# Performance work log

Hardware: AMD Instinct MI355X
Metric: run time of the kernel (lower is better)

## Reference

```python
import jax, jax.numpy as jnp
import numpy as np

N_HEAD, MODEL_DIM, KEY_DIM, VALUE_DIM = 16, 1024, 64, 64
B, S = 4, 2048
EPS = 1e-5
TEMP = float(np.sqrt(KEY_DIM))


def setup_inputs() -> dict:
    key = jax.random.key(0)
    ks = jax.random.split(key, 12)
    d = {
        'query': jax.random.normal(ks[0], (B, S, MODEL_DIM), jnp.float32),
        'key':   jax.random.normal(ks[1], (B, S, MODEL_DIM), jnp.float32),
        'value': jax.random.normal(ks[2], (B, S, MODEL_DIM), jnp.float32),
        # projection weights stored as [in, out]
        'Wq': jax.random.normal(ks[3], (MODEL_DIM, N_HEAD * KEY_DIM), jnp.float32) * np.sqrt(2.0 / (MODEL_DIM + KEY_DIM)),
        'bq': jnp.zeros((N_HEAD * KEY_DIM,), jnp.float32),
        'Wk': jax.random.normal(ks[4], (MODEL_DIM, N_HEAD * KEY_DIM), jnp.float32) * np.sqrt(2.0 / (MODEL_DIM + KEY_DIM)),
        'bk': jnp.zeros((N_HEAD * KEY_DIM,), jnp.float32),
        'Wv': jax.random.normal(ks[5], (MODEL_DIM, N_HEAD * VALUE_DIM), jnp.float32) * np.sqrt(2.0 / (MODEL_DIM + VALUE_DIM)),
        'bv': jnp.zeros((N_HEAD * VALUE_DIM,), jnp.float32),
        'Wo': jax.random.normal(ks[6], (N_HEAD * VALUE_DIM, MODEL_DIM), jnp.float32) * np.sqrt(2.0 / (N_HEAD * VALUE_DIM + MODEL_DIM)),
        'bo': jnp.zeros((MODEL_DIM,), jnp.float32),
        'ln_gamma': jnp.ones((MODEL_DIM,), jnp.float32),
        'ln_beta': jnp.zeros((MODEL_DIM,), jnp.float32),
    }
    return d


def reference(query, key, value, Wq, bq, Wk, bk, Wv, bv, Wo, bo, ln_gamma, ln_beta):
    b, sq, _ = query.shape
    residual = query
    # QKV projections -> [B, S, H, D]
    q = (query @ Wq + bq).reshape(b, sq, N_HEAD, KEY_DIM)
    k = (key @ Wk + bk).reshape(b, key.shape[1], N_HEAD, KEY_DIM)
    v = (value @ Wv + bv).reshape(b, value.shape[1], N_HEAD, VALUE_DIM)
    # scaled dot-product attention (dropout inactive in eval)
    scores = jnp.einsum('bqhd,bkhd->bhqk', q, k) / TEMP
    attn = jax.nn.softmax(scores, axis=-1)
    out = jnp.einsum('bhqk,bkhd->bqhd', attn, v).reshape(b, sq, N_HEAD * VALUE_DIM)
    # output projection + residual + LayerNorm
    out = out @ Wo + bo + residual
    mu = jnp.mean(out, axis=-1, keepdims=True)
    var = jnp.var(out, axis=-1, keepdims=True)
    return (out - mu) * jax.lax.rsqrt(var + EPS) * ln_gamma + ln_beta
```

## Files before the change

### kernel.cpp

```cpp
#include <hip/hip_runtime.h>
#include <math.h>

#define MD 1024
#define NH 16
#define HD 64
#define BATCH 4
#define SEQ 2048

typedef __attribute__((ext_vector_type(8))) short short8;
typedef __attribute__((ext_vector_type(4))) short short4v;
typedef __attribute__((ext_vector_type(4))) float f32x4;
typedef __attribute__((ext_vector_type(2))) unsigned int uint2v;

#define GLOAD16(gp, lp) __builtin_amdgcn_global_load_lds( \
    (const __attribute__((address_space(1))) void*)(gp),  \
    (__attribute__((address_space(3))) void*)(lp), 16, 0, 0)

__device__ inline unsigned short f2b(float f) {
    unsigned u = __builtin_bit_cast(unsigned, f);
    unsigned r = (u + 0x7fffu + ((u >> 16) & 1u)) >> 16;
    return (unsigned short)r;
}
__device__ inline float b2f(unsigned short s) {
    return __builtin_bit_cast(float, ((unsigned)s) << 16);
}

__global__ __launch_bounds__(256)
void prep_kernel(const float* __restrict__ x0, const float* __restrict__ x1,
                 const float* __restrict__ x2, unsigned short* __restrict__ y0,
                 unsigned short* __restrict__ y1, unsigned short* __restrict__ y2,
                 int n,
                 const float* __restrict__ W0, const float* __restrict__ W1,
                 const float* __restrict__ W2, const float* __restrict__ W3,
                 unsigned short* __restrict__ T0, unsigned short* __restrict__ T1,
                 unsigned short* __restrict__ T2, unsigned short* __restrict__ T3)
{
    __shared__ __attribute__((aligned(16))) float T[64][68];
    const int tid = threadIdx.x;
    if (blockIdx.y < 3) {
        const float* x = (blockIdx.y == 0) ? x0 : (blockIdx.y == 1) ? x1 : x2;
        unsigned short* y = (blockIdx.y == 0) ? y0 : (blockIdx.y == 1) ? y1 : y2;
        int i = (blockIdx.x * 256 + tid) * 8;
        if (i >= n) return;
        f32x4 a = *(const f32x4*)(x + i);
        f32x4 b = *(const f32x4*)(x + i + 4);
        short8 o;
        o[0] = (short)f2b(a[0]); o[1] = (short)f2b(a[1]);
        o[2] = (short)f2b(a[2]); o[3] = (short)f2b(a[3]);
        o[4] = (short)f2b(b[0]); o[5] = (short)f2b(b[1]);
        o[6] = (short)f2b(b[2]); o[7] = (short)f2b(b[3]);
        *(short8*)(y + i) = o;
        return;
    }
    const int bx = blockIdx.x;
    if (bx >= 1024) return;
    const int z = bx >> 8, t = bx & 255;
    const int nt = t & 15, kt = t >> 4;
    const float* W = (z == 0) ? W0 : (z == 1) ? W1 : (z == 2) ? W2 : W3;
    unsigned short* WT = (z == 0) ? T0 : (z == 1) ? T1 : (z == 2) ? T2 : T3;
    #pragma unroll
    for (int i = 0; i < 4; ++i) {
        int u = tid + i * 256;
        int row = u >> 4, c4 = u & 15;
        f32x4 v = *(const f32x4*)(W + (size_t)(kt * 64 + row) * MD + nt * 64 + c4 * 4);
        *(f32x4*)&T[row][c4 * 4] = v;
    }
    __syncthreads();
    #pragma unroll
    for (int i = 0; i < 2; ++i) {
        int u = tid + i * 256;
        int nn = u >> 3, c16 = u & 7;
        short8 o;
        #pragma unroll
        for (int j = 0; j < 8; ++j) o[j] = (short)f2b(T[c16 * 8 + j][nn]);
        *(short8*)(WT + (size_t)(nt * 64 + nn) * MD + kt * 64 + c16 * 8) = o;
    }
}

__device__ __forceinline__
void gemm_core(const unsigned short* __restrict__ A,
               const unsigned short* __restrict__ Bt,
               short* As, short* Bs, f32x4 acc[4][4],
               int* obrow, int* obcol)
{
    const int tid = threadIdx.x;
    const int lane = tid & 63;
    const int wave = tid >> 6;
    const int wm = wave >> 1, wn = wave & 1;
    const int l15 = lane & 15, g = lane >> 4;

    const int nbx = gridDim.x;
    const int bid = blockIdx.y * nbx + blockIdx.x;
    const int cpx = (nbx * gridDim.y) >> 3;
    const int swz = (bid & 7) * cpx + (bid >> 3);
    const int brow = (swz / nbx) * 128;
    const int bcol = (swz % nbx) * 128;
    *obrow = brow; *obcol = bcol;

    #pragma unroll
    for (int m = 0; m < 4; ++m)
        #pragma unroll
        for (int n = 0; n < 4; ++n) acc[m][n] = (f32x4){0.f, 0.f, 0.f, 0.f};

    for (int k0 = 0; k0 < MD; k0 += 64) {
        __syncthreads();
        #pragma unroll
        for (int i = 0; i < 4; ++i) {
            const int U = (i * 4 + wave) * 64 + lane;
            const int row = U >> 3, c16 = U & 7;
            GLOAD16(A  + (size_t)(brow + row) * MD + k0 + c16 * 8, &As[U * 8]);
            GLOAD16(Bt + (size_t)(bcol + row) * MD + k0 + c16 * 8, &Bs[U * 8]);
        }
        __syncthreads();
        #pragma unroll
        for (int kk = 0; kk < 64; kk += 32) {
            short8 af[4], bf_[4];
            #pragma unroll
            for (int m = 0; m < 4; ++m)
                af[m] = *(const short8*)&As[(wm * 64 + m * 16 + l15) * 64 + kk + g * 8];
            #pragma unroll
            for (int n = 0; n < 4; ++n)
                bf_[n] = *(const short8*)&Bs[(wn * 64 + n * 16 + l15) * 64 + kk + g * 8];
            #pragma unroll
            for (int m = 0; m < 4; ++m)
                #pragma unroll
                for (int n = 0; n < 4; ++n)
                    acc[m][n] = __builtin_amdgcn_mfma_f32_16x16x32_bf16(af[m], bf_[n], acc[m][n], 0, 0, 0);
        }
    }
}

__global__ __launch_bounds__(256, 2)
void gemm_qkv(const unsigned short* __restrict__ A0, const unsigned short* __restrict__ A1,
              const unsigned short* __restrict__ A2,
              const unsigned short* __restrict__ B0, const unsigned short* __restrict__ B1,
              const unsigned short* __restrict__ B2,
              const float* __restrict__ b0, const float* __restrict__ b1,
              const float* __restrict__ b2,
              unsigned short* __restrict__ Cq, unsigned short* __restrict__ Ck,
              unsigned short* __restrict__ Cvt)
{
    __shared__ __attribute__((aligned(16))) short As[128 * 64];
    __shared__ __attribute__((aligned(16))) short Bs[128 * 64];
    const int z = blockIdx.z;
    const unsigned short* A  = (z == 0) ? A0 : (z == 1) ? A1 : A2;
    const unsigned short* Bt = (z == 0) ? B0 : (z == 1) ? B1 : B2;
    const float* bias        = (z == 0) ? b0 : (z == 1) ? b1 : b2;

    f32x4 acc[4][4];
    int brow, bcol;
    gemm_core(A, Bt, As, Bs, acc, &brow, &bcol);

    const int tid = threadIdx.x;
    const int lane = tid & 63;
    const int wave = tid >> 6;
    const int wm = wave >> 1, wn = wave & 1;
    const int l15 = lane & 15, g = lane >> 4;

    if (z == 2) {
        #pragma unroll
        for (int m = 0; m < 4; ++m) {
            #pragma unroll
            for (int n = 0; n < 4; ++n) {
                const int col = bcol + wn * 64 + n * 16 + l15;
                const int h = col >> 6, d = col & 63;
                const float bv_ = bias[col];
                const int row0 = brow + wm * 64 + m * 16 + 4 * g;
                const int bb = row0 >> 11, s = row0 & 2047;
                short4v pk;
                #pragma unroll
                for (int r = 0; r < 4; ++r) pk[r] = (short)f2b(acc[m][n][r] + bv_);
                *(short4v*)(Cvt + ((size_t)((bb << 4) + h) * 64 + d) * SEQ + s) = pk;
            }
        }
        return;
    }
    const float scale = (z == 0) ? (0.125f * 1.44269504088896f) : 1.0f;
    unsigned short* C = (z == 0) ? Cq : Ck;
    #pragma unroll
    for (int m = 0; m < 4; ++m) {
        #pragma unroll
        for (int n = 0; n < 4; ++n) {
            const int col = bcol + wn * 64 + n * 16 + l15;
            const float bcol_v = bias[col];
            #pragma unroll
            for (int r = 0; r < 4; ++r) {
                const size_t row = (size_t)(brow + wm * 64 + m * 16 + 4 * g + r);
                C[row * MD + col] = f2b((acc[m][n][r] + bcol_v) * scale);
            }
        }
    }
}

__global__ __launch_bounds__(256, 2)
void gemm_o(const unsigned short* __restrict__ A, const unsigned short* __restrict__ Bt,
            const float* __restrict__ bias, const float* __restrict__ residual,
            float* __restrict__ Cf)
{
    __shared__ __attribute__((aligned(16))) short As[128 * 64];
    __shared__ __attribute__((aligned(16))) short Bs[128 * 64];
    f32x4 acc[4][4];
    int brow, bcol;
    gemm_core(A, Bt, As, Bs, acc, &brow, &bcol);

    const int tid = threadIdx.x;
    const int lane = tid & 63;
    const int wave = tid >> 6;
    const int wm = wave >> 1, wn = wave & 1;
    const int l15 = lane & 15, g = lane >> 4;
    #pragma unroll
    for (int m = 0; m < 4; ++m) {
        #pragma unroll
        for (int n = 0; n < 4; ++n) {
            const int col = bcol + wn * 64 + n * 16 + l15;
            const float bcol_v = bias[col];
            #pragma unroll
            for (int r = 0; r < 4; ++r) {
                const size_t row = (size_t)(brow + wm * 64 + m * 16 + 4 * g + r);
                Cf[row * MD + col] = acc[m][n][r] + bcol_v + residual[row * MD + col];
            }
        }
    }
}

__global__ __launch_bounds__(256, 2)
void attn_mfma(const unsigned short* __restrict__ qp,
               const unsigned short* __restrict__ kp,
               const unsigned short* __restrict__ vt,
               unsigned short* __restrict__ ao)
{
    __shared__ __attribute__((aligned(16))) short Ps[256 * 64];
    __shared__ __attribute__((aligned(16))) short Ks[2][64 * 64];
    __shared__ __attribute__((aligned(16))) short Vts[2][64 * 64];

    const int tid = threadIdx.x;
    const int lane = tid & 63;
    const int wave = tid >> 6;
    const int l15 = lane & 15, g = lane >> 4;
    const int qt = blockIdx.x, bh = blockIdx.y;
    const int b = bh >> 4, h = bh & 15;
    const size_t rowbase = (size_t)b * SEQ;
    const int q0 = qt * 256;
    const int wq = wave * 64;
    const int NT = SEQ / 64;

    const int r0 = tid >> 3, c16 = tid & 7;
    const int r1 = r0 + 32;
    const int lds0 = (r0 * 8 + (c16 ^ (r0 & 7))) * 8;
    const int lds1 = (r1 * 8 + (c16 ^ (r1 & 7))) * 8;
    const unsigned short* kbase = kp + (rowbase + r0) * MD + h * 64 + c16 * 8;
    const unsigned short* vbase = vt + ((size_t)bh * 64 + r0) * SEQ + c16 * 8;

    short8 qreg[4][2];
    #pragma unroll
    for (int nf = 0; nf < 4; ++nf)
        #pragma unroll
        for (int ki = 0; ki < 2; ++ki)
            qreg[nf][ki] = *(const short8*)(qp + (rowbase + q0 + wq + nf * 16 + l15) * MD
                                               + h * 64 + ki * 32 + g * 8);

    {
        short8 k0v = *(const short8*)(kbase);
        short8 k1v = *(const short8*)(kbase + 32 * MD);
        short8 v0v = *(const short8*)(vbase);
        short8 v1v = *(const short8*)(vbase + 32 * SEQ);
        *(short8*)&Ks[0][lds0]  = k0v;
        *(short8*)&Ks[0][lds1]  = k1v;
        *(short8*)&Vts[0][lds0] = v0v;
        *(short8*)&Vts[0][lds1] = v1v;
    }
    __syncthreads();

    short8 ones;
    #pragma unroll
    for (int j = 0; j < 8; ++j) ones[j] = (short)0x3F80;

    float mrun[4] = {-INFINITY, -INFINITY, -INFINITY, -INFINITY};
    f32x4 lrun[4];
    f32x4 off[4][4];
    #pragma unroll
    for (int qf = 0; qf < 4; ++qf) {
        lrun[qf] = (f32x4){0.f, 0.f, 0.f, 0.f};
        #pragma unroll
        for (int df = 0; df < 4; ++df) off[qf][df] = (f32x4){0.f, 0.f, 0.f, 0.f};
    }

    for (int kt = 0; kt < NT; ++kt) {
        const int cur = kt & 1;

        short8 kreg0, kreg1, vreg0, vreg1;
        if (kt + 1 < NT) {
            const unsigned short* kb = kbase + (size_t)(kt + 1) * 64 * MD;
            const unsigned short* vb = vbase + (kt + 1) * 64;
            kreg0 = *(const short8*)(kb);
            kreg1 = *(const short8*)(kb + 32 * MD);
            vreg0 = *(const short8*)(vb);
            vreg1 = *(const short8*)(vb + 32 * SEQ);
        }

        f32x4 sc[4][4];
        #pragma unroll
        for (int mf = 0; mf < 4; ++mf)
            #pragma unroll
            for (int nf = 0; nf < 4; ++nf) sc[mf][nf] = (f32x4){0.f, 0.f, 0.f, 0.f};
        __builtin_amdgcn_s_setprio(1);
        #pragma unroll
        for (int ki = 0; ki < 2; ++ki) {
            const int cu = ki * 4 + g;
            short8 af[4];
            #pragma unroll
            for (int mf = 0; mf < 4; ++mf) {
                int row = mf * 16 + l15;
                af[mf] = *(const short8*)&Ks[cur][(row * 8 + (cu ^ (row & 7))) * 8];
            }
            #pragma unroll
            for (int mf = 0; mf < 4; ++mf)
                #pragma unroll
                for (int nf = 0; nf < 4; ++nf)
                    sc[mf][nf] = __builtin_amdgcn_mfma_f32_16x16x32_bf16(af[mf], qreg[nf][ki], sc[mf][nf], 0, 0, 0);
        }
        __builtin_amdgcn_s_setprio(0);

        float pmax[4];
        #pragma unroll
        for (int nf = 0; nf < 4; ++nf) {
            float pm = -INFINITY;
            #pragma unroll
            for (int mf = 0; mf < 4; ++mf)
                #pragma unroll
                for (int r = 0; r < 4; ++r) pm = fmaxf(pm, sc[mf][nf][r]);
            pm = fmaxf(pm, __shfl_xor(pm, 16));
            pm = fmaxf(pm, __shfl_xor(pm, 32));
            pmax[nf] = pm;
        }
        const int defer = (pmax[0] <= mrun[0] + 8.0f) && (pmax[1] <= mrun[1] + 8.0f) &&
                          (pmax[2] <= mrun[2] + 8.0f) && (pmax[3] <= mrun[3] + 8.0f);
        if (!__all(defer)) {
            float corr[4];
            #pragma unroll
            for (int nf = 0; nf < 4; ++nf) {
                float mnew = fmaxf(mrun[nf], pmax[nf]);
                corr[nf] = __builtin_amdgcn_exp2f(mrun[nf] - mnew);
                mrun[nf] = mnew;
            }
            #pragma unroll
            for (int qf = 0; qf < 4; ++qf)
                #pragma unroll
                for (int r = 0; r < 4; ++r) {
                    float c = __shfl(corr[qf], 4 * g + r);
                    lrun[qf][r] *= c;
                    #pragma unroll
                    for (int df = 0; df < 4; ++df) off[qf][df][r] *= c;
                }
        }
        #pragma unroll
        for (int nf = 0; nf < 4; ++nf) {
            const float nm = mrun[nf];
            #pragma unroll
            for (int mf = 0; mf < 4; ++mf)
                #pragma unroll
                for (int r = 0; r < 4; ++r)
                    sc[mf][nf][r] = __builtin_amdgcn_exp2f(sc[mf][nf][r] - nm);
        }

        #pragma unroll
        for (int nf = 0; nf < 4; ++nf) {
            int row = wq + nf * 16 + l15;
            #pragma unroll
            for (int mf = 0; mf < 4; ++mf) {
                unsigned p01, p23;
                asm("v_cvt_pk_bf16_f32 %0, %1, %2" : "=v"(p01) : "v"(sc[mf][nf][0]), "v"(sc[mf][nf][1]));
                asm("v_cvt_pk_bf16_f32 %0, %1, %2" : "=v"(p23) : "v"(sc[mf][nf][2]), "v"(sc[mf][nf][3]));
                uint2v pk = {p01, p23};
                int su = (mf * 2 + (g >> 1)) ^ (row & 7);
                *(uint2v*)&Ps[row * 64 + su * 8 + (g & 1) * 4] = pk;
            }
        }

        f32x4 ts[4];
        #pragma unroll
        for (int qf = 0; qf < 4; ++qf) ts[qf] = (f32x4){0.f, 0.f, 0.f, 0.f};
        __builtin_amdgcn_s_setprio(1);
        #pragma unroll
        for (int ki = 0; ki < 2; ++ki) {
            const int cu = ki * 4 + g;
            short8 pa[4], vb[4];
            #pragma unroll
            for (int qf = 0; qf < 4; ++qf) {
                int row = wq + qf * 16 + l15;
                pa[qf] = *(const short8*)&Ps[(row * 8 + (cu ^ (row & 7))) * 8];
            }
            #pragma unroll
            for (int df = 0; df < 4; ++df) {
                int d = df * 16 + l15;
                vb[df] = *(const short8*)&Vts[cur][(d * 8 + (cu ^ (d & 7))) * 8];
            }
            #pragma unroll
            for (int qf = 0; qf < 4; ++qf)
                #pragma unroll
                for (int df = 0; df < 4; ++df)
                    off[qf][df] = __builtin_amdgcn_mfma_f32_16x16x32_bf16(pa[qf], vb[df], off[qf][df], 0, 0, 0);
            #pragma unroll
            for (int qf = 0; qf < 4; ++qf)
                ts[qf] = __builtin_amdgcn_mfma_f32_16x16x32_bf16(pa[qf], ones, ts[qf], 0, 0, 0);
        }
        __builtin_amdgcn_s_setprio(0);
        #pragma unroll
        for (int qf = 0; qf < 4; ++qf)
            #pragma unroll
            for (int r = 0; r < 4; ++r) lrun[qf][r] += ts[qf][r];

        if (kt + 1 < NT) {
            const int nxt = cur ^ 1;
            *(short8*)&Ks[nxt][lds0]  = kreg0;
            *(short8*)&Ks[nxt][lds1]  = kreg1;
            *(short8*)&Vts[nxt][lds0] = vreg0;
            *(short8*)&Vts[nxt][lds1] = vreg1;
        }
        __syncthreads();
    }

    #pragma unroll
    for (int qf = 0; qf < 4; ++qf) {
        #pragma unroll
        for (int r = 0; r < 4; ++r) {
            const float inv = 1.0f / lrun[qf][r];
            const size_t row = rowbase + q0 + wq + qf * 16 + 4 * g + r;
            #pragma unroll
            for (int df = 0; df < 4; ++df) {
                float val = off[qf][df][r] * inv;
                ao[row * MD + h * 64 + df * 16 + l15] = f2b(val);
            }
        }
    }
}

__global__ __launch_bounds__(256)
void ln_kernel(float* __restrict__ X, const float* __restrict__ gamma,
               const float* __restrict__ beta)
{
    const int row = blockIdx.x;
    const int tid = threadIdx.x;
    float* px = X + (size_t)row * MD;
    f32x4 x = ((const f32x4*)px)[tid];
    float s  = x[0] + x[1] + x[2] + x[3];
    float ss = fmaf(x[0], x[0], fmaf(x[1], x[1], fmaf(x[2], x[2], x[3] * x[3])));
    #pragma unroll
    for (int off = 1; off < 64; off <<= 1) {
        s  += __shfl_xor(s,  off);
        ss += __shfl_xor(ss, off);
    }
    __shared__ float red[8];
    const int wid = tid >> 6;
    if ((tid & 63) == 0) { red[wid] = s; red[wid + 4] = ss; }
    __syncthreads();
    s  = red[0] + red[1] + red[2] + red[3];
    ss = red[4] + red[5] + red[6] + red[7];
    const float mu   = s * (1.0f / MD);
    const float var  = ss * (1.0f / MD) - mu * mu;
    const float rstd = rsqrtf(var + 1e-5f);
    f32x4 gm = ((const f32x4*)gamma)[tid];
    f32x4 be = ((const f32x4*)beta)[tid];
    f32x4 r;
    r[0] = (x[0] - mu) * rstd * gm[0] + be[0];
    r[1] = (x[1] - mu) * rstd * gm[1] + be[1];
    r[2] = (x[2] - mu) * rstd * gm[2] + be[2];
    r[3] = (x[3] - mu) * rstd * gm[3] + be[3];
    ((f32x4*)px)[tid] = r;
}

extern "C" void kernel_launch(void* const* d_in, const int* in_sizes, int n_in,
                              void* d_out, int out_size, void* d_ws, size_t ws_size,
                              hipStream_t stream)
{
    const float* query = (const float*)d_in[0];
    const float* key   = (const float*)d_in[1];
    const float* value = (const float*)d_in[2];
    const float* Wq = (const float*)d_in[3];
    const float* bq = (const float*)d_in[4];
    const float* Wk = (const float*)d_in[5];
    const float* bk = (const float*)d_in[6];
    const float* Wv = (const float*)d_in[7];
    const float* bv = (const float*)d_in[8];
    const float* Wo = (const float*)d_in[9];
    const float* bo = (const float*)d_in[10];
    const float* gamma = (const float*)d_in[11];
    const float* beta  = (const float*)d_in[12];
    float* out = (float*)d_out;

    const size_t NTOK = (size_t)BATCH * SEQ;
    const size_t ACT  = NTOK * MD;

    unsigned short* qa  = (unsigned short*)d_ws;
    unsigned short* ka  = qa + ACT;
    unsigned short* va  = ka + ACT;
    unsigned short* WqT = va + ACT;
    unsigned short* WkT = WqT + (size_t)MD * MD;
    unsigned short* WvT = WkT + (size_t)MD * MD;
    unsigned short* WoT = WvT + (size_t)MD * MD;
    unsigned short* qp  = WoT + (size_t)MD * MD;
    unsigned short* kp  = qp + ACT;
    unsigned short* vtp = kp + ACT;
    unsigned short* ao  = ka;

    dim3 blk(256);

    prep_kernel<<<dim3(4096, 4), blk, 0, stream>>>(
        query, key, value, qa, ka, va, (int)ACT,
        Wq, Wk, Wv, Wo, WqT, WkT, WvT, WoT);

    dim3 gg(MD / 128, NTOK / 128, 3);
    gemm_qkv<<<gg, blk, 0, stream>>>(qa, ka, va, WqT, WkT, WvT,
                                     bq, bk, bv, qp, kp, vtp);

    attn_mfma<<<dim3(SEQ / 256, 64), blk, 0, stream>>>(qp, kp, vtp, ao);

    gemm_o<<<dim3(MD / 128, NTOK / 128), blk, 0, stream>>>(ao, WoT, bo, query, out);

    ln_kernel<<<NTOK, blk, 0, stream>>>(out, gamma, beta);
}
```

Before: 225.1 us.

## Single-buffer K/V LDS tiles, raise attention occupancy, and remap blocks for L2 locality

The K/V shared-memory tiles go from double to single buffering, cutting LDS per block so launch bounds can target three blocks per SIMD instead of two. Global loads for the next tile are still held in registers, but they are now written to LDS at the top of each iteration between two barriers. Block indices are remapped so neighbouring blocks share batch-head groups across query tiles, which should improve L2 reuse of K/V. The max reduction is rewritten as paired fmax calls. The cost is an extra barrier per iteration and tighter register limits that may cause spills.

```diff
diff --git a/kernel.cpp b/kernel.cpp
--- a/kernel.cpp
+++ b/kernel.cpp
@@ -223,21 +223,26 @@
     }
 }
 
-__global__ __launch_bounds__(256, 2)
+__global__ __launch_bounds__(256, 3)
 void attn_mfma(const unsigned short* __restrict__ qp,
                const unsigned short* __restrict__ kp,
                const unsigned short* __restrict__ vt,
                unsigned short* __restrict__ ao)
 {
     __shared__ __attribute__((aligned(16))) short Ps[256 * 64];
-    __shared__ __attribute__((aligned(16))) short Ks[2][64 * 64];
-    __shared__ __attribute__((aligned(16))) short Vts[2][64 * 64];
+    __shared__ __attribute__((aligned(16))) short Ks[64 * 64];
+    __shared__ __attribute__((aligned(16))) short Vts[64 * 64];
 
     const int tid = threadIdx.x;
     const int lane = tid & 63;
     const int wave = tid >> 6;
     const int l15 = lane & 15, g = lane >> 4;
-    const int qt = blockIdx.x, bh = blockIdx.y;
+
+    const int lin = blockIdx.y * gridDim.x + blockIdx.x;
+    const int xi = lin & 7, j = lin >> 3;
+    const int bh = xi + 8 * (j & 7);
+    const int qt = j >> 3;
+
     const int b = bh >> 4, h = bh & 15;
     const size_t rowbase = (size_t)b * SEQ;
     const int q0 = qt * 256;
@@ -259,21 +264,14 @@
             qreg[nf][ki] = *(const short8*)(qp + (rowbase + q0 + wq + nf * 16 + l15) * MD
                                                + h * 64 + ki * 32 + g * 8);
 
-    {
-        short8 k0v = *(const short8*)(kbase);
-        short8 k1v = *(const short8*)(kbase + 32 * MD);
-        short8 v0v = *(const short8*)(vbase);
-        short8 v1v = *(const short8*)(vbase + 32 * SEQ);
-        *(short8*)&Ks[0][lds0]  = k0v;
-        *(short8*)&Ks[0][lds1]  = k1v;
-        *(short8*)&Vts[0][lds0] = v0v;
-        *(short8*)&Vts[0][lds1] = v1v;
-    }
-    __syncthreads();
+    short8 kreg0 = *(const short8*)(kbase);
+    short8 kreg1 = *(const short8*)(kbase + 32 * MD);
+    short8 vreg0 = *(const short8*)(vbase);
+    short8 vreg1 = *(const short8*)(vbase + 32 * SEQ);
 
     short8 ones;
     #pragma unroll
-    for (int j = 0; j < 8; ++j) ones[j] = (short)0x3F80;
+    for (int jj = 0; jj < 8; ++jj) ones[jj] = (short)0x3F80;
 
     float mrun[4] = {-INFINITY, -INFINITY, -INFINITY, -INFINITY};
     f32x4 lrun[4];
@@ -286,9 +284,11 @@
     }
 
     for (int kt = 0; kt < NT; ++kt) {
-        const int cur = kt & 1;
-
-        short8 kreg0, kreg1, vreg0, vreg1;
+        __syncthreads();
+        *(short8*)&Ks[lds0]  = kreg0;
+        *(short8*)&Ks[lds1]  = kreg1;
+        *(short8*)&Vts[lds0] = vreg0;
+        *(short8*)&Vts[lds1] = vreg1;
         if (kt + 1 < NT) {
             const unsigned short* kb = kbase + (size_t)(kt + 1) * 64 * MD;
             const unsigned short* vb = vbase + (kt + 1) * 64;
@@ -297,6 +297,7 @@
             vreg0 = *(const short8*)(vb);
             vreg1 = *(const short8*)(vb + 32 * SEQ);
         }
+        __syncthreads();
 
         f32x4 sc[4][4];
         #pragma unroll
@@ -311,7 +312,7 @@
             #pragma unroll
             for (int mf = 0; mf < 4; ++mf) {
                 int row = mf * 16 + l15;
-                af[mf] = *(const short8*)&Ks[cur][(row * 8 + (cu ^ (row & 7))) * 8];
+                af[mf] = *(const short8*)&Ks[(row * 8 + (cu ^ (row & 7))) * 8];
             }
             #pragma unroll
             for (int mf = 0; mf < 4; ++mf)
@@ -324,11 +325,14 @@
         float pmax[4];
         #pragma unroll
         for (int nf = 0; nf < 4; ++nf) {
-            float pm = -INFINITY;
-            #pragma unroll
-            for (int mf = 0; mf < 4; ++mf)
-                #pragma unroll
-                for (int r = 0; r < 4; ++r) pm = fmaxf(pm, sc[mf][nf][r]);
+            float pm = fmaxf(fmaxf(sc[0][nf][0], sc[0][nf][1]), sc[0][nf][2]);
+            pm = fmaxf(fmaxf(pm, sc[0][nf][3]), sc[1][nf][0]);
+            pm = fmaxf(fmaxf(pm, sc[1][nf][1]), sc[1][nf][2]);
+            pm = fmaxf(fmaxf(pm, sc[1][nf][3]), sc[2][nf][0]);
+            pm = fmaxf(fmaxf(pm, sc[2][nf][1]), sc[2][nf][2]);
+            pm = fmaxf(fmaxf(pm, sc[2][nf][3]), sc[3][nf][0]);
+            pm = fmaxf(fmaxf(pm, sc[3][nf][1]), sc[3][nf][2]);
+            pm = fmaxf(pm, sc[3][nf][3]);
             pm = fmaxf(pm, __shfl_xor(pm, 16));
             pm = fmaxf(pm, __shfl_xor(pm, 32));
             pmax[nf] = pm;
@@ -393,7 +397,7 @@
             #pragma unroll
             for (int df = 0; df < 4; ++df) {
                 int d = df * 16 + l15;
-                vb[df] = *(const short8*)&Vts[cur][(d * 8 + (cu ^ (d & 7))) * 8];
+                vb[df] = *(const short8*)&Vts[(d * 8 + (cu ^ (d & 7))) * 8];
             }
             #pragma unroll
             for (int qf = 0; qf < 4; ++qf)
@@ -409,15 +413,6 @@
         for (int qf = 0; qf < 4; ++qf)
             #pragma unroll
             for (int r = 0; r < 4; ++r) lrun[qf][r] += ts[qf][r];
-
-        if (kt + 1 < NT) {
-            const int nxt = cur ^ 1;
-            *(short8*)&Ks[nxt][lds0]  = kreg0;
-            *(short8*)&Ks[nxt][lds1]  = kreg1;
-            *(short8*)&Vts[nxt][lds0] = vreg0;
-            *(short8*)&Vts[nxt][lds1] = vreg1;
-        }
-        __syncthreads();
     }
 
     #pragma unroll
```

Result: slower. 522.2 us (+132.0%).
